# Kernel optimization log

Hardware: AMD Instinct MI355X
Metric: run time of the kernel (lower is better)

Reference implementation:

```python
import jax, jax.numpy as jnp
import numpy as np

DIM = 1024
HEADS = 16
DIM_HEAD = 64
WINDOW = 256  # sliding window size == block size
NEG = -1e9


def rms_norm(x, gamma, size):
    # F.normalize(x, dim=-1) * sqrt(size) * gamma
    nrm = jnp.sqrt(jnp.sum(x * x, axis=-1, keepdims=True))
    return x / jnp.maximum(nrm, 1e-12) * (size ** 0.5) * gamma


def sliding_window_attention(q, k, v, window):
    # q,k,v: [b, h, S, d]; causal local attention: key j valid iff i-window <= j <= i
    b, h, S, d = q.shape
    Bk = window
    nb = S // Bk
    qb = q.reshape(b, h, nb, Bk, d)
    kb = k.reshape(b, h, nb, Bk, d)
    vb = v.reshape(b, h, nb, Bk, d)
    # previous key/value block (zeros for block 0; masked out below)
    k_prev = jnp.pad(kb, ((0, 0), (0, 0), (1, 0), (0, 0), (0, 0)))[:, :, :nb]
    v_prev = jnp.pad(vb, ((0, 0), (0, 0), (1, 0), (0, 0), (0, 0)))[:, :, :nb]
    kctx = jnp.concatenate([k_prev, kb], axis=3)  # [b,h,nb,2Bk,d]
    vctx = jnp.concatenate([v_prev, vb], axis=3)
    scale = 1.0 / jnp.sqrt(jnp.asarray(d, q.dtype))
    scores = jnp.einsum('bhnqd,bhnkd->bhnqk', qb, kctx) * scale  # [b,h,nb,Bk,2Bk]
    qi = jnp.arange(Bk)[:, None]          # local query index
    kj = jnp.arange(2 * Bk)[None, :]      # local key index (offset -Bk rel to block start)
    diff = Bk + qi - kj                   # global i - j
    base = (diff >= 0) & (diff <= window)  # [Bk, 2Bk]
    blk = jnp.arange(nb)[:, None, None]
    key_exists = ((blk - 1) * Bk + kj[None]) >= 0  # [nb,1,2Bk] -> broadcast
    mask = base[None] & key_exists                 # [nb,Bk,2Bk]
    scores = jnp.where(mask[None, None], scores, NEG)
    attn = jax.nn.softmax(scores, axis=-1)
    out = jnp.einsum('bhnqk,bhnkd->bhnqd', attn, vctx)
    return out.reshape(b, h, S, d)


def setup_inputs() -> dict:
    key = jax.random.key(0)
    ks = jax.random.split(key, 6)
    b, S = 2, 4096
    dim_inner = HEADS * DIM_HEAD
    x = jax.random.normal(ks[0], (b, S, DIM), dtype=jnp.float32)
    gamma = jnp.ones((DIM,), dtype=jnp.float32)
    W_qkv = jax.random.normal(ks[1], (DIM, 3 * dim_inner), dtype=jnp.float32) * 0.02
    W_gates = jax.random.normal(ks[2], (DIM, HEADS), dtype=jnp.float32) * 0.02
    b_gates = jnp.zeros((HEADS,), dtype=jnp.float32)
    W_out = jax.random.normal(ks[3], (dim_inner, DIM), dtype=jnp.float32) * 0.02
    return {"x": x, "gamma": gamma, "W_qkv": W_qkv, "W_gates": W_gates,
            "b_gates": b_gates, "W_out": W_out}


def reference(x, gamma, W_qkv, W_gates, b_gates, W_out):
    b, S, dim = x.shape
    xn = rms_norm(x, gamma, dim)
    qkv = xn @ W_qkv                                    # [b,S,3*h*d]
    qkv = qkv.reshape(b, S, 3, HEADS, DIM_HEAD)
    q, k, v = [jnp.transpose(t, (0, 2, 1, 3)) for t in
               (qkv[:, :, 0], qkv[:, :, 1], qkv[:, :, 2])]  # [b,h,S,d]
    out = sliding_window_attention(q, k, v, WINDOW)      # [b,h,S,d]
    gates = xn @ W_gates + b_gates                       # [b,S,h]
    out = out * jax.nn.sigmoid(jnp.transpose(gates, (0, 2, 1)))[..., None]
    out = jnp.transpose(out, (0, 2, 1, 3)).reshape(b, S, HEADS * DIM_HEAD)
    return out @ W_out
```

## Files before the change

### kernel.cpp

```cpp
#include <hip/hip_runtime.h>
#include <hip/hip_bf16.h>
#include <stdint.h>

typedef __bf16 bf16;
typedef __bf16 bf16x4 __attribute__((ext_vector_type(4)));
typedef __bf16 bf16x8 __attribute__((ext_vector_type(8)));
typedef float f32x4 __attribute__((ext_vector_type(4)));

#define GLOBAL_AS __attribute__((address_space(1)))
#define LDS_AS __attribute__((address_space(3)))

__device__ __forceinline__ void g2lds16(const bf16* g, bf16* l) {
  __builtin_amdgcn_global_load_lds((const GLOBAL_AS void*)g, (LDS_AS void*)l, 16, 0, 0);
}

__global__ __launch_bounds__(256) void rmsnorm_kernel(
    const float* __restrict__ x, const float* __restrict__ gamma,
    bf16* __restrict__ xn) {
  __shared__ float wss[4];
  const int t = threadIdx.x;
  const size_t row = blockIdx.x;
  const float* xr = x + row * 1024;

  float4 xv = *(const float4*)&xr[t * 4];
  float v[4] = {xv.x, xv.y, xv.z, xv.w};
  float ss = v[0]*v[0] + v[1]*v[1] + v[2]*v[2] + v[3]*v[3];
#pragma unroll
  for (int mm = 1; mm < 64; mm <<= 1) ss += __shfl_xor(ss, mm);
  if ((t & 63) == 0) wss[t >> 6] = ss;
  __syncthreads();
  ss = wss[0] + wss[1] + wss[2] + wss[3];
  float inv = 32.0f / sqrtf(fmaxf(ss, 1e-24f));

  float4 gv = *(const float4*)&gamma[t * 4];
  float gvv[4] = {gv.x, gv.y, gv.z, gv.w};
  bf16x4 outv;
#pragma unroll
  for (int i = 0; i < 4; ++i) outv[i] = (bf16)(v[i] * inv * gvv[i]);
  *(bf16x4*)&xn[row * 1024 + t * 4] = outv;
}

__global__ void transpose_f32_bf16(const float* __restrict__ in, bf16* __restrict__ out,
                                   int R, int C) {
  __shared__ bf16 tile[32][33];
  const int tx = threadIdx.x, ty = threadIdx.y;
  const int c0 = blockIdx.x * 32, r0 = blockIdx.y * 32;
#pragma unroll
  for (int i = 0; i < 32; i += 8)
    tile[ty + i][tx] = (bf16)in[(size_t)(r0 + ty + i) * C + c0 + tx];
  __syncthreads();
#pragma unroll
  for (int i = 0; i < 32; i += 8)
    out[(size_t)(c0 + ty + i) * R + r0 + tx] = tile[tx][ty + i];
}

__global__ __launch_bounds__(256) void wg_transpose(const float* __restrict__ Wg,
                                                    bf16* __restrict__ BtAug) {
  int idx = blockIdx.x * 256 + threadIdx.x;
  int n = idx >> 10, k = idx & 1023;
  BtAug[(size_t)(3072 + n) * 1024 + k] = (bf16)Wg[(size_t)k * 16 + n];
}

template <typename OutT>
__global__ __launch_bounds__(256) void gemm_bt_128(
    const bf16* __restrict__ A, const bf16* __restrict__ Bt,
    OutT* __restrict__ C, int M, int N, int K) {
  __shared__ bf16 lA[128 * 64];
  __shared__ bf16 lB[128 * 64];
  const int t = threadIdx.x;
  const int w = t >> 6, lane = t & 63;
  const int col0 = lane & 15, quad = lane >> 4;
  const int m0 = blockIdx.y * 128, n0 = blockIdx.x * 128;
  const int wr = (w >> 1) * 64, wc = (w & 1) * 64;

  const int lrow = t >> 3;
  const int sswz = (((t & 7) ^ (lrow & 7)) << 3);

  f32x4 acc[4][4] = {};

  for (int k0 = 0; k0 < K; k0 += 64) {
    __syncthreads();
#pragma unroll
    for (int c = 0; c < 4; ++c) {
      g2lds16(A  + (size_t)(m0 + c * 32 + lrow) * K + k0 + sswz, &lA[c * 2048 + w * 512]);
      g2lds16(Bt + (size_t)(n0 + c * 32 + lrow) * K + k0 + sswz, &lB[c * 2048 + w * 512]);
    }
    __syncthreads();

#pragma unroll
    for (int kh = 0; kh < 2; ++kh) {
      bf16x8 af[4], bfr[4];
#pragma unroll
      for (int i = 0; i < 4; ++i) {
        int row = wr + i * 16 + col0;
        af[i] = *(const bf16x8*)&lA[row * 64 + (((kh * 4 + quad) ^ (row & 7)) << 3)];
      }
#pragma unroll
      for (int j = 0; j < 4; ++j) {
        int row = wc + j * 16 + col0;
        bfr[j] = *(const bf16x8*)&lB[row * 64 + (((kh * 4 + quad) ^ (row & 7)) << 3)];
      }
#pragma unroll
      for (int i = 0; i < 4; ++i)
#pragma unroll
        for (int j = 0; j < 4; ++j)
          acc[i][j] = __builtin_amdgcn_mfma_f32_16x16x32_bf16(af[i], bfr[j], acc[i][j], 0, 0, 0);
    }
  }

#pragma unroll
  for (int i = 0; i < 4; ++i)
#pragma unroll
    for (int j = 0; j < 4; ++j)
#pragma unroll
      for (int r = 0; r < 4; ++r) {
        int row = m0 + wr + i * 16 + quad * 4 + r;
        int col = n0 + wc + j * 16 + col0;
        C[(size_t)row * N + col] = (OutT)acc[i][j][r];
      }
}

template <typename OutT>
__global__ __launch_bounds__(512, 2) void gemm_bt_256(
    const bf16* __restrict__ A, const bf16* __restrict__ Bt,
    OutT* __restrict__ C, int M, int N, int K) {
  extern __shared__ bf16 lds[];
  bf16* A0 = lds;
  bf16* B0 = lds + 16384;
  bf16* A1 = lds + 32768;
  bf16* B1 = lds + 49152;

  const int t = threadIdx.x;
  const int w = t >> 6, lane = t & 63;
  const int wm = w >> 2, wn = w & 3;
  const int col0 = lane & 15, quad = lane >> 4;
  const int sswz = (((t & 7) ^ ((t >> 3) & 7)) << 3);

  int nwg = gridDim.x * gridDim.y;
  int bid = blockIdx.y * gridDim.x + blockIdx.x;
  int swz = bid;
  if ((nwg & 7) == 0) swz = (bid & 7) * (nwg >> 3) + (bid >> 3);
  const int n0 = (swz % gridDim.x) * 256;
  const int m0 = (swz / gridDim.x) * 256;

  const bf16* Abase = A + (size_t)m0 * (size_t)K;

  auto stageA = [&](int ks, int c, bf16* dstA) {
    int row = c * 64 + (t >> 3);
    g2lds16(Abase + (size_t)row * K + ks + sswz, dstA + c * 4096 + w * 512);
  };
  auto stageB = [&](int ks, int c, bf16* dstB) {
    int gr = n0 + c * 64 + (t >> 3);
    gr = (gr < N) ? gr : (N - 1);
    g2lds16(Bt + (size_t)gr * (size_t)K + ks + sswz, dstB + c * 4096 + w * 512);
  };

  f32x4 acc[4][2][4] = {};
  const int NT = K >> 6;

  stageB(0, 0, B0); stageB(0, 1, B0); stageB(0, 2, B0); stageB(0, 3, B0);
  stageA(0, 0, A0);
  stageA(0, 1, A0); stageA(0, 2, A0); stageA(0, 3, A0);
  asm volatile("s_waitcnt vmcnt(3)" ::: "memory");
  __builtin_amdgcn_s_barrier();

  for (int T = 0; T < NT; ++T) {
    bf16* cA = (T & 1) ? A1 : A0;
    bf16* cB = (T & 1) ? B1 : B0;
    bf16* nA = (T & 1) ? A0 : A1;
    bf16* nB = (T & 1) ? B0 : B1;
    int tn = T + 1;
    int kn = ((tn < NT) ? tn : 0) << 6;

    bf16x8 bv[4][2];
#pragma unroll
    for (int q = 0; q < 4; ++q) {
      if (q == 0) {
#pragma unroll
        for (int nj = 0; nj < 4; ++nj) {
          int br = wn * 64 + nj * 16 + col0;
#pragma unroll
          for (int ks = 0; ks < 2; ++ks)
            bv[nj][ks] = *(const bf16x8*)&cB[br * 64 + (((ks * 4 + quad) ^ (br & 7)) << 3)];
        }
      }
      bf16x8 af[2][2];
#pragma unroll
      for (int m2 = 0; m2 < 2; ++m2) {
        int ar = q * 64 + wm * 32 + m2 * 16 + col0;
#pragma unroll
        for (int ks = 0; ks < 2; ++ks)
          af[m2][ks] = *(const bf16x8*)&cA[ar * 64 + (((ks * 4 + quad) ^ (ar & 7)) << 3)];
      }
      if (q == 0)      { stageA(kn, 0, nA); stageB(kn, 0, nB); }
      else if (q == 1) { stageB(kn, 1, nB); stageB(kn, 2, nB); }
      else if (q == 2) { stageB(kn, 3, nB); stageA(kn, 1, nA); }
      else             { stageA(kn, 2, nA); stageA(kn, 3, nA); }
      if (q == 0)      asm volatile("s_waitcnt vmcnt(4)" ::: "memory");
      else if (q == 1) asm volatile("s_waitcnt vmcnt(5)" ::: "memory");
      else if (q == 2) asm volatile("s_waitcnt vmcnt(6)" ::: "memory");
      else             asm volatile("s_waitcnt vmcnt(3)" ::: "memory");
      __builtin_amdgcn_s_barrier();
      asm volatile("s_waitcnt lgkmcnt(0)" ::: "memory");
      __builtin_amdgcn_sched_barrier(0);
      __builtin_amdgcn_s_setprio(1);
#pragma unroll
      for (int ks = 0; ks < 2; ++ks)
#pragma unroll
        for (int m2 = 0; m2 < 2; ++m2)
#pragma unroll
          for (int nj = 0; nj < 4; ++nj)
            acc[q][m2][nj] = __builtin_amdgcn_mfma_f32_16x16x32_bf16(
                af[m2][ks], bv[nj][ks], acc[q][m2][nj], 0, 0, 0);
      __builtin_amdgcn_s_setprio(0);
      __builtin_amdgcn_s_barrier();
    }
  }
  asm volatile("s_waitcnt vmcnt(0)" ::: "memory");

#pragma unroll
  for (int q = 0; q < 4; ++q)
#pragma unroll
    for (int m2 = 0; m2 < 2; ++m2)
#pragma unroll
      for (int nj = 0; nj < 4; ++nj) {
        int col = n0 + wn * 64 + nj * 16 + col0;
        if (col < N) {
          size_t base = (size_t)(m0 + q * 64 + wm * 32 + m2 * 16 + quad * 4) * N + col;
#pragma unroll
          for (int r = 0; r < 4; ++r)
            C[base + (size_t)r * N] = (OutT)acc[q][m2][nj][r];
        }
      }
}

#define NEG_BIG -1e30f
__global__ __launch_bounds__(256, 4) void attn_kernel(
    const bf16* __restrict__ qkv, const float* __restrict__ bg,
    bf16* __restrict__ attnO) {
  __shared__ bf16 lKV[320 * 64];

  const int t = threadIdx.x;
  const int lane = t & 63;
  const int w = t >> 6;
  const int col0 = lane & 15, quad = lane >> 4;

  const int bid = blockIdx.x;
  const int blk = ((bid & 7) << 8) | (bid >> 3);
  const int g = blk & 63;
  const int h = (blk >> 6) & 15;
  const int bb = blk >> 10;
  const int qs = g * 64;

  const size_t rs = 3200;
  const bf16* qbase = qkv + ((size_t)bb * 4096) * rs + h * 64;

  {
    const int lr = t >> 3;
    const int sswz = ((t & 7) ^ (lr & 7)) << 3;
#pragma unroll
    for (int c = 0; c < 10; ++c) {
      int j = qs - 256 + c * 32 + lr;
      j = (j < 0) ? 0 : j;
      g2lds16(qbase + 1024 + (size_t)j * rs + sswz, &lKV[c * 2048 + w * 512]);
    }
  }
  __builtin_amdgcn_sched_barrier(0);
  const int ql = w * 16 + col0;
  const int srow = qs + ql;
  const bf16x8 bq0 = *(const bf16x8*)(qbase + (size_t)srow * rs + quad * 8);
  const bf16x8 bq1 = *(const bf16x8*)(qbase + (size_t)srow * rs + 32 + quad * 8);
  const float logit = (float)qkv[((size_t)bb * 4096 + srow) * rs + 3072 + h];
  asm volatile("s_waitcnt vmcnt(3)" ::: "memory");
  asm volatile("s_barrier" ::: "memory");

  f32x4 z[20];
#pragma unroll
  for (int kt = 0; kt < 20; ++kt) {
    const int kr = kt * 16 + col0;
    bf16x8 a0 = *(const bf16x8*)&lKV[kr * 64 + ((quad ^ (kr & 7)) << 3)];
    bf16x8 a1 = *(const bf16x8*)&lKV[kr * 64 + (((4 + quad) ^ (kr & 7)) << 3)];
    f32x4 zz = {};
    zz = __builtin_amdgcn_mfma_f32_16x16x32_bf16(a0, bq0, zz, 0, 0, 0);
    zz = __builtin_amdgcn_mfma_f32_16x16x32_bf16(a1, bq1, zz, 0, 0, 0);
    z[kt] = zz;
  }
  asm volatile("s_barrier" ::: "memory");

  {
    const int jl = t & 31, dg = t >> 5;
#pragma unroll
    for (int cc = 0; cc < 10; ++cc) {
      int j = qs - 256 + cc * 32 + jl;
      j = (j < 0) ? 0 : j;
      bf16 tmp[8];
      *(uint4*)tmp = *(const uint4*)(qbase + 2048 + (size_t)j * rs + dg * 8);
      const int ck = cc * 4 + (jl >> 3);
      const int wi = jl & 7;
#pragma unroll
      for (int d2 = 0; d2 < 8; ++d2) {
        const int d = dg * 8 + d2;
        lKV[d * 320 + ((ck ^ (d & 7)) << 3) + wi] = tmp[d2];
      }
    }
  }

  float m = NEG_BIG;
#pragma unroll
  for (int kt = 0; kt < 20; ++kt)
#pragma unroll
    for (int r = 0; r < 4; ++r) {
      const int c = kt * 16 + quad * 4 + r;
      const bool valid = (c >= ql) && (c <= ql + 256) && (qs - 256 + c >= 0);
      const float sv = valid ? z[kt][r] * 0.125f : NEG_BIG;
      z[kt][r] = sv;
      m = fmaxf(m, sv);
    }
  m = fmaxf(m, __shfl_xor(m, 16));
  m = fmaxf(m, __shfl_xor(m, 32));
  float l = 0.f;
#pragma unroll
  for (int kt = 0; kt < 20; ++kt)
#pragma unroll
    for (int r = 0; r < 4; ++r) {
      const float p = __expf(z[kt][r] - m);
      z[kt][r] = p;
      l += p;
    }
  l += __shfl_xor(l, 16);
  l += __shfl_xor(l, 32);

  __syncthreads();

  f32x4 o[4] = {};
  const int sl0 = col0 + ((quad & 1) << 5);
  const bool hi = quad >= 2;
#pragma unroll
  for (int kc = 0; kc < 10; ++kc) {
    uint32_t Pl0, Pl1, Ph0, Ph1;
    asm("v_cvt_pk_bf16_f32 %0, %1, %2" : "=v"(Pl0) : "v"(z[2*kc][0]),   "v"(z[2*kc][1]));
    asm("v_cvt_pk_bf16_f32 %0, %1, %2" : "=v"(Pl1) : "v"(z[2*kc][2]),   "v"(z[2*kc][3]));
    asm("v_cvt_pk_bf16_f32 %0, %1, %2" : "=v"(Ph0) : "v"(z[2*kc+1][0]), "v"(z[2*kc+1][1]));
    asm("v_cvt_pk_bf16_f32 %0, %1, %2" : "=v"(Ph1) : "v"(z[2*kc+1][2]), "v"(z[2*kc+1][3]));
    uint32_t w0l = __shfl((int)Pl0, sl0),      w0h = __shfl((int)Ph0, sl0);
    uint32_t w1l = __shfl((int)Pl1, sl0),      w1h = __shfl((int)Ph1, sl0);
    uint32_t w2l = __shfl((int)Pl0, sl0 + 16), w2h = __shfl((int)Ph0, sl0 + 16);
    uint32_t w3l = __shfl((int)Pl1, sl0 + 16), w3h = __shfl((int)Ph1, sl0 + 16);
    union { uint32_t u[4]; bf16x8 v; } pu;
    pu.u[0] = hi ? w0h : w0l;
    pu.u[1] = hi ? w1h : w1l;
    pu.u[2] = hi ? w2h : w2l;
    pu.u[3] = hi ? w3h : w3l;
#pragma unroll
    for (int n = 0; n < 4; ++n) {
      const int d = n * 16 + col0;
      bf16x8 av = *(const bf16x8*)&lKV[d * 320 + (((kc * 4 + quad) ^ (d & 7)) << 3)];
      o[n] = __builtin_amdgcn_mfma_f32_16x16x32_bf16(av, pu.v, o[n], 0, 0, 0);
    }
  }

  const float gate = 1.f / (1.f + __expf(-(logit + bg[h])));
  const float scale = gate / l;
  bf16* obase = attnO + ((size_t)bb * 4096 + srow) * 1024 + h * 64;
#pragma unroll
  for (int n = 0; n < 4; ++n) {
    bf16x4 ov;
#pragma unroll
    for (int r = 0; r < 4; ++r) ov[r] = (bf16)(o[n][r] * scale);
    *(bf16x4*)&obase[n * 16 + quad * 4] = ov;
  }
}

extern "C" void kernel_launch(void* const* d_in, const int* in_sizes, int n_in,
                              void* d_out, int out_size, void* d_ws, size_t ws_size,
                              hipStream_t stream) {
  const float *x = nullptr, *gamma = nullptr, *Wqkv = nullptr,
              *Wg = nullptr, *bg = nullptr, *Wout = nullptr;
  for (int i = 0; i < n_in; ++i) {
    switch (in_sizes[i]) {
      case 8388608: x     = (const float*)d_in[i]; break;
      case 1024:    gamma = (const float*)d_in[i]; break;
      case 3145728: Wqkv  = (const float*)d_in[i]; break;
      case 16384:   Wg    = (const float*)d_in[i]; break;
      case 16:      bg    = (const float*)d_in[i]; break;
      case 1048576: Wout  = (const float*)d_in[i]; break;
    }
  }
  float* out = (float*)d_out;

  static bool attr_done = false;
  if (!attr_done) {
    hipFuncSetAttribute(reinterpret_cast<const void*>(&gemm_bt_256<bf16>),
                        hipFuncAttributeMaxDynamicSharedMemorySize, 131072);
    attr_done = true;
  }

  char* ws = (char*)d_ws;
  bf16* qkv   = (bf16*)ws;  ws += (size_t)8192 * 3200 * 2;
  bf16* xn    = (bf16*)ws;
  bf16* attnO = (bf16*)ws;  ws += (size_t)8192 * 1024 * 2;
  bf16* BtAug = (bf16*)ws;  ws += (size_t)3200 * 1024 * 2;
  bf16* WoutT = (bf16*)ws;  ws += (size_t)1024 * 1024 * 2;

  hipMemsetAsync(BtAug + (size_t)3088 * 1024, 0, (size_t)112 * 1024 * 2, stream);

  rmsnorm_kernel<<<8192, 256, 0, stream>>>(x, gamma, xn);
  transpose_f32_bf16<<<dim3(3072 / 32, 1024 / 32), dim3(32, 8), 0, stream>>>(Wqkv, BtAug, 1024, 3072);
  wg_transpose<<<64, 256, 0, stream>>>(Wg, BtAug);
  transpose_f32_bf16<<<dim3(1024 / 32, 1024 / 32), dim3(32, 8), 0, stream>>>(Wout, WoutT, 1024, 1024);
  gemm_bt_256<bf16><<<dim3(13, 32), 512, 131072, stream>>>(xn, BtAug, qkv, 8192, 3200, 1024);
  attn_kernel<<<2048, 256, 0, stream>>>(qkv, bg, attnO);
  gemm_bt_128<float><<<dim3(1024 / 128, 8192 / 128), 256, 0, stream>>>(attnO, WoutT, out, 8192, 1024, 1024);
}
```

Measured before the change: 235.1 us.

## Load B fragments directly from global to registers, stage only A in LDS

The QKV GEMM no longer stages the B (weight) tile through LDS. Each wave reads its B fragments straight from global memory into registers, and only the A tile stays double-buffered in static LDS (64 KB instead of 128 KB dynamic). This cuts LDS footprint and LDS traffic for B, drops per-quarter barriers, and simplifies the pipeline to one wait and barrier per K step. The trade-off is uncached-by-LDS global loads for B, which are redundantly read by waves sharing columns, and a full vmcnt(0) wait that exposes load latency.

```diff
diff --git a/kernel.cpp b/kernel.cpp
--- a/kernel.cpp
+++ b/kernel.cpp
@@ -124,11 +124,7 @@
 __global__ __launch_bounds__(512, 2) void gemm_bt_256(
     const bf16* __restrict__ A, const bf16* __restrict__ Bt,
     OutT* __restrict__ C, int M, int N, int K) {
-  extern __shared__ bf16 lds[];
-  bf16* A0 = lds;
-  bf16* B0 = lds + 16384;
-  bf16* A1 = lds + 32768;
-  bf16* B1 = lds + 49152;
+  __shared__ bf16 lA[2][256 * 64];
 
   const int t = threadIdx.x;
   const int w = t >> 6, lane = t & 63;
@@ -149,60 +145,51 @@
     int row = c * 64 + (t >> 3);
     g2lds16(Abase + (size_t)row * K + ks + sswz, dstA + c * 4096 + w * 512);
   };
-  auto stageB = [&](int ks, int c, bf16* dstB) {
-    int gr = n0 + c * 64 + (t >> 3);
+
+  const bf16* brow[4];
+#pragma unroll
+  for (int nj = 0; nj < 4; ++nj) {
+    int gr = n0 + wn * 64 + nj * 16 + col0;
     gr = (gr < N) ? gr : (N - 1);
-    g2lds16(Bt + (size_t)gr * (size_t)K + ks + sswz, dstB + c * 4096 + w * 512);
-  };
+    brow[nj] = Bt + (size_t)gr * (size_t)K + quad * 8;
+  }
 
   f32x4 acc[4][2][4] = {};
   const int NT = K >> 6;
 
-  stageB(0, 0, B0); stageB(0, 1, B0); stageB(0, 2, B0); stageB(0, 3, B0);
-  stageA(0, 0, A0);
-  stageA(0, 1, A0); stageA(0, 2, A0); stageA(0, 3, A0);
-  asm volatile("s_waitcnt vmcnt(3)" ::: "memory");
-  __builtin_amdgcn_s_barrier();
+  stageA(0, 0, lA[0]); stageA(0, 1, lA[0]); stageA(0, 2, lA[0]); stageA(0, 3, lA[0]);
 
   for (int T = 0; T < NT; ++T) {
-    bf16* cA = (T & 1) ? A1 : A0;
-    bf16* cB = (T & 1) ? B1 : B0;
-    bf16* nA = (T & 1) ? A0 : A1;
-    bf16* nB = (T & 1) ? B0 : B1;
-    int tn = T + 1;
-    int kn = ((tn < NT) ? tn : 0) << 6;
+    bf16* cur = lA[T & 1];
+    bf16* nxt = lA[(T + 1) & 1];
+    const int k0 = T << 6;
+
+    asm volatile("s_waitcnt vmcnt(0)" ::: "memory");
+    asm volatile("s_barrier" ::: "memory");
 
     bf16x8 bv[4][2];
 #pragma unroll
+    for (int nj = 0; nj < 4; ++nj)
+#pragma unroll
+      for (int ks = 0; ks < 2; ++ks)
+        bv[nj][ks] = *(const bf16x8*)(brow[nj] + k0 + ks * 32);
+    __builtin_amdgcn_sched_barrier(0);
+
+    if (T + 1 < NT) {
+      const int kn = (T + 1) << 6;
+      stageA(kn, 0, nxt); stageA(kn, 1, nxt); stageA(kn, 2, nxt); stageA(kn, 3, nxt);
+    }
+
+#pragma unroll
     for (int q = 0; q < 4; ++q) {
-      if (q == 0) {
-#pragma unroll
-        for (int nj = 0; nj < 4; ++nj) {
-          int br = wn * 64 + nj * 16 + col0;
-#pragma unroll
-          for (int ks = 0; ks < 2; ++ks)
-            bv[nj][ks] = *(const bf16x8*)&cB[br * 64 + (((ks * 4 + quad) ^ (br & 7)) << 3)];
-        }
-      }
       bf16x8 af[2][2];
 #pragma unroll
       for (int m2 = 0; m2 < 2; ++m2) {
         int ar = q * 64 + wm * 32 + m2 * 16 + col0;
 #pragma unroll
         for (int ks = 0; ks < 2; ++ks)
-          af[m2][ks] = *(const bf16x8*)&cA[ar * 64 + (((ks * 4 + quad) ^ (ar & 7)) << 3)];
-      }
-      if (q == 0)      { stageA(kn, 0, nA); stageB(kn, 0, nB); }
-      else if (q == 1) { stageB(kn, 1, nB); stageB(kn, 2, nB); }
-      else if (q == 2) { stageB(kn, 3, nB); stageA(kn, 1, nA); }
-      else             { stageA(kn, 2, nA); stageA(kn, 3, nA); }
-      if (q == 0)      asm volatile("s_waitcnt vmcnt(4)" ::: "memory");
-      else if (q == 1) asm volatile("s_waitcnt vmcnt(5)" ::: "memory");
-      else if (q == 2) asm volatile("s_waitcnt vmcnt(6)" ::: "memory");
-      else             asm volatile("s_waitcnt vmcnt(3)" ::: "memory");
-      __builtin_amdgcn_s_barrier();
-      asm volatile("s_waitcnt lgkmcnt(0)" ::: "memory");
-      __builtin_amdgcn_sched_barrier(0);
+          af[m2][ks] = *(const bf16x8*)&cur[ar * 64 + (((ks * 4 + quad) ^ (ar & 7)) << 3)];
+      }
       __builtin_amdgcn_s_setprio(1);
 #pragma unroll
       for (int ks = 0; ks < 2; ++ks)
@@ -213,7 +200,6 @@
             acc[q][m2][nj] = __builtin_amdgcn_mfma_f32_16x16x32_bf16(
                 af[m2][ks], bv[nj][ks], acc[q][m2][nj], 0, 0, 0);
       __builtin_amdgcn_s_setprio(0);
-      __builtin_amdgcn_s_barrier();
     }
   }
   asm volatile("s_waitcnt vmcnt(0)" ::: "memory");
@@ -388,13 +374,6 @@
   }
   float* out = (float*)d_out;
 
-  static bool attr_done = false;
-  if (!attr_done) {
-    hipFuncSetAttribute(reinterpret_cast<const void*>(&gemm_bt_256<bf16>),
-                        hipFuncAttributeMaxDynamicSharedMemorySize, 131072);
-    attr_done = true;
-  }
-
   char* ws = (char*)d_ws;
   bf16* qkv   = (bf16*)ws;  ws += (size_t)8192 * 3200 * 2;
   bf16* xn    = (bf16*)ws;
@@ -408,7 +387,7 @@
   transpose_f32_bf16<<<dim3(3072 / 32, 1024 / 32), dim3(32, 8), 0, stream>>>(Wqkv, BtAug, 1024, 3072);
   wg_transpose<<<64, 256, 0, stream>>>(Wg, BtAug);
   transpose_f32_bf16<<<dim3(1024 / 32, 1024 / 32), dim3(32, 8), 0, stream>>>(Wout, WoutT, 1024, 1024);
-  gemm_bt_256<bf16><<<dim3(13, 32), 512, 131072, stream>>>(xn, BtAug, qkv, 8192, 3200, 1024);
+  gemm_bt_256<bf16><<<dim3(13, 32), 512, 0, stream>>>(xn, BtAug, qkv, 8192, 3200, 1024);
   attn_kernel<<<2048, 256, 0, stream>>>(qkv, bg, attnO);
   gemm_bt_128<float><<<dim3(1024 / 128, 8192 / 128), 256, 0, stream>>>(attnO, WoutT, out, 8192, 1024, 1024);
 }
```

After: 270.5 us. 15.0% more time.

## Replace output GEMM with pipelined 256x128 kernel and restructure QKV GEMM warp tiling

Applied to the files above, without the earlier changes.

Drops the simple 128x128 output-projection GEMM in favour of a new 256x128, 512-thread kernel with double-buffered direct-to-LDS loads, grid swizzling and staged vmcnt waits. The QKV GEMM's warp layout changes so each warp owns 128 rows by 64 columns instead of four 32-row strips, with new per-warp staging addresses and the K loop unrolled by two over the buffers. The aim is better data reuse and overlap of global loads with MFMA work. The hand-placed waitcnt and barrier ordering is delicate and could add stalls or produce wrong results if the counts are off.

```diff
diff --git a/kernel.cpp b/kernel.cpp
--- a/kernel.cpp
+++ b/kernel.cpp
@@ -59,65 +59,6 @@
   int idx = blockIdx.x * 256 + threadIdx.x;
   int n = idx >> 10, k = idx & 1023;
   BtAug[(size_t)(3072 + n) * 1024 + k] = (bf16)Wg[(size_t)k * 16 + n];
-}
-
-template <typename OutT>
-__global__ __launch_bounds__(256) void gemm_bt_128(
-    const bf16* __restrict__ A, const bf16* __restrict__ Bt,
-    OutT* __restrict__ C, int M, int N, int K) {
-  __shared__ bf16 lA[128 * 64];
-  __shared__ bf16 lB[128 * 64];
-  const int t = threadIdx.x;
-  const int w = t >> 6, lane = t & 63;
-  const int col0 = lane & 15, quad = lane >> 4;
-  const int m0 = blockIdx.y * 128, n0 = blockIdx.x * 128;
-  const int wr = (w >> 1) * 64, wc = (w & 1) * 64;
-
-  const int lrow = t >> 3;
-  const int sswz = (((t & 7) ^ (lrow & 7)) << 3);
-
-  f32x4 acc[4][4] = {};
-
-  for (int k0 = 0; k0 < K; k0 += 64) {
-    __syncthreads();
-#pragma unroll
-    for (int c = 0; c < 4; ++c) {
-      g2lds16(A  + (size_t)(m0 + c * 32 + lrow) * K + k0 + sswz, &lA[c * 2048 + w * 512]);
-      g2lds16(Bt + (size_t)(n0 + c * 32 + lrow) * K + k0 + sswz, &lB[c * 2048 + w * 512]);
-    }
-    __syncthreads();
-
-#pragma unroll
-    for (int kh = 0; kh < 2; ++kh) {
-      bf16x8 af[4], bfr[4];
-#pragma unroll
-      for (int i = 0; i < 4; ++i) {
-        int row = wr + i * 16 + col0;
-        af[i] = *(const bf16x8*)&lA[row * 64 + (((kh * 4 + quad) ^ (row & 7)) << 3)];
-      }
-#pragma unroll
-      for (int j = 0; j < 4; ++j) {
-        int row = wc + j * 16 + col0;
-        bfr[j] = *(const bf16x8*)&lB[row * 64 + (((kh * 4 + quad) ^ (row & 7)) << 3)];
-      }
-#pragma unroll
-      for (int i = 0; i < 4; ++i)
-#pragma unroll
-        for (int j = 0; j < 4; ++j)
-          acc[i][j] = __builtin_amdgcn_mfma_f32_16x16x32_bf16(af[i], bfr[j], acc[i][j], 0, 0, 0);
-    }
-  }
-
-#pragma unroll
-  for (int i = 0; i < 4; ++i)
-#pragma unroll
-    for (int j = 0; j < 4; ++j)
-#pragma unroll
-      for (int r = 0; r < 4; ++r) {
-        int row = m0 + wr + i * 16 + quad * 4 + r;
-        int col = n0 + wc + j * 16 + col0;
-        C[(size_t)row * N + col] = (OutT)acc[i][j][r];
-      }
 }
 
 template <typename OutT>
@@ -134,7 +75,8 @@
   const int w = t >> 6, lane = t & 63;
   const int wm = w >> 2, wn = w & 3;
   const int col0 = lane & 15, quad = lane >> 4;
-  const int sswz = (((t & 7) ^ ((t >> 3) & 7)) << 3);
+  const int s_sub = lane >> 3;
+  const int sswz = (((lane & 7) ^ s_sub) << 3);
 
   int nwg = gridDim.x * gridDim.y;
   int bid = blockIdx.y * gridDim.x + blockIdx.x;
@@ -146,19 +88,155 @@
   const bf16* Abase = A + (size_t)m0 * (size_t)K;
 
   auto stageA = [&](int ks, int c, bf16* dstA) {
+    int rb = (w < 4) ? (c * 32 + w * 8) : (128 + c * 32 + (w - 4) * 8);
+    g2lds16(Abase + (size_t)(rb + s_sub) * K + ks + sswz, dstA + rb * 64);
+  };
+  auto stageB = [&](int ks, int c, bf16* dstB) {
+    int rb = c * 64 + w * 8;
+    int gr = n0 + rb + s_sub;
+    gr = (gr < N) ? gr : (N - 1);
+    g2lds16(Bt + (size_t)gr * (size_t)K + ks + sswz, dstB + rb * 64);
+  };
+
+  f32x4 acc[8][4] = {};
+  const int NT = K >> 6;
+  const int NI = NT >> 1;
+
+#pragma unroll
+  for (int c = 0; c < 4; ++c) stageB(0, c, B0);
+  stageA(0, 0, A0);
+  stageA(0, 1, A0); stageA(0, 2, A0); stageA(0, 3, A0);
+  asm volatile("s_waitcnt vmcnt(3)" ::: "memory");
+  __builtin_amdgcn_s_barrier();
+
+  for (int i = 0; i < NI; ++i) {
+#pragma unroll
+    for (int h = 0; h < 2; ++h) {
+      bf16* cA = h ? A1 : A0;
+      bf16* cB = h ? B1 : B0;
+      bf16* nA = h ? A0 : A1;
+      bf16* nB = h ? B0 : B1;
+      int tn = 2 * i + h + 1;
+      int kn = ((tn < NT) ? tn : 0) << 6;
+
+      bf16x8 bv[4][2];
+#pragma unroll
+      for (int nj = 0; nj < 4; ++nj) {
+        int br = wn * 64 + nj * 16 + col0;
+#pragma unroll
+        for (int ks = 0; ks < 2; ++ks)
+          bv[nj][ks] = *(const bf16x8*)&cB[br * 64 + (((ks * 4 + quad) ^ (br & 7)) << 3)];
+      }
+      {
+        bf16x8 af[2][2];
+#pragma unroll
+        for (int m2 = 0; m2 < 2; ++m2) {
+          int ar = wm * 128 + m2 * 16 + col0;
+#pragma unroll
+          for (int ks = 0; ks < 2; ++ks)
+            af[m2][ks] = *(const bf16x8*)&cA[ar * 64 + (((ks * 4 + quad) ^ (ar & 7)) << 3)];
+        }
+        stageB(kn, 0, nB); stageB(kn, 1, nB);
+        __builtin_amdgcn_s_barrier();
+        asm volatile("s_waitcnt lgkmcnt(0)" ::: "memory");
+        __builtin_amdgcn_s_setprio(1);
+#pragma unroll
+        for (int ks = 0; ks < 2; ++ks)
+#pragma unroll
+          for (int m2 = 0; m2 < 2; ++m2)
+#pragma unroll
+            for (int nj = 0; nj < 4; ++nj)
+              acc[m2][nj] = __builtin_amdgcn_mfma_f32_16x16x32_bf16(
+                  af[m2][ks], bv[nj][ks], acc[m2][nj], 0, 0, 0);
+        __builtin_amdgcn_s_setprio(0);
+        asm volatile("s_waitcnt vmcnt(4)" ::: "memory");
+        __builtin_amdgcn_s_barrier();
+      }
+
+#pragma unroll
+      for (int p = 1; p < 4; ++p) {
+        bf16x8 af[2][2];
+#pragma unroll
+        for (int m2 = 0; m2 < 2; ++m2) {
+          int ar = wm * 128 + (p * 2 + m2) * 16 + col0;
+#pragma unroll
+          for (int ks = 0; ks < 2; ++ks)
+            af[m2][ks] = *(const bf16x8*)&cA[ar * 64 + (((ks * 4 + quad) ^ (ar & 7)) << 3)];
+        }
+        if (p == 1)      { stageB(kn, 2, nB); stageB(kn, 3, nB); stageA(kn, 0, nA); }
+        else if (p == 2) { stageA(kn, 1, nA); stageA(kn, 2, nA); }
+        else             { stageA(kn, 3, nA); }
+        __builtin_amdgcn_s_barrier();
+        asm volatile("s_waitcnt lgkmcnt(0)" ::: "memory");
+        __builtin_amdgcn_s_setprio(1);
+#pragma unroll
+        for (int ks = 0; ks < 2; ++ks)
+#pragma unroll
+          for (int m2 = 0; m2 < 2; ++m2)
+#pragma unroll
+            for (int nj = 0; nj < 4; ++nj)
+              acc[p * 2 + m2][nj] = __builtin_amdgcn_mfma_f32_16x16x32_bf16(
+                  af[m2][ks], bv[nj][ks], acc[p * 2 + m2][nj], 0, 0, 0);
+        __builtin_amdgcn_s_setprio(0);
+        if (p == 1)      asm volatile("s_waitcnt vmcnt(6)" ::: "memory");
+        else if (p == 2) asm volatile("s_waitcnt vmcnt(7)" ::: "memory");
+        else             asm volatile("s_waitcnt vmcnt(3)" ::: "memory");
+        __builtin_amdgcn_s_barrier();
+      }
+    }
+  }
+  asm volatile("s_waitcnt vmcnt(0)" ::: "memory");
+
+#pragma unroll
+  for (int mi = 0; mi < 8; ++mi)
+#pragma unroll
+    for (int nj = 0; nj < 4; ++nj) {
+      int col = n0 + wn * 64 + nj * 16 + col0;
+      if (col < N) {
+        size_t base = (size_t)(m0 + wm * 128 + mi * 16 + quad * 4) * N + col;
+#pragma unroll
+        for (int r = 0; r < 4; ++r)
+          C[base + (size_t)r * N] = (OutT)acc[mi][nj][r];
+      }
+    }
+}
+
+__global__ __launch_bounds__(512, 2) void gemm_out_256x128(
+    const bf16* __restrict__ A, const bf16* __restrict__ Bt,
+    float* __restrict__ C, int M, int N, int K) {
+  extern __shared__ bf16 lds[];
+  bf16* A0 = lds;
+  bf16* B0 = lds + 16384;
+  bf16* A1 = lds + 24576;
+  bf16* B1 = lds + 40960;
+
+  const int t = threadIdx.x;
+  const int w = t >> 6, lane = t & 63;
+  const int wm = w >> 2, wn = w & 3;
+  const int col0 = lane & 15, quad = lane >> 4;
+  const int sswz = (((t & 7) ^ ((t >> 3) & 7)) << 3);
+
+  int nwg = gridDim.x * gridDim.y;
+  int bid = blockIdx.y * gridDim.x + blockIdx.x;
+  int swz = (bid & 7) * (nwg >> 3) + (bid >> 3);
+  const int n0 = (swz % gridDim.x) * 128;
+  const int m0 = (swz / gridDim.x) * 256;
+
+  const bf16* Abase = A + (size_t)m0 * (size_t)K;
+
+  auto stageA = [&](int ks, int c, bf16* dstA) {
     int row = c * 64 + (t >> 3);
     g2lds16(Abase + (size_t)row * K + ks + sswz, dstA + c * 4096 + w * 512);
   };
   auto stageB = [&](int ks, int c, bf16* dstB) {
     int gr = n0 + c * 64 + (t >> 3);
-    gr = (gr < N) ? gr : (N - 1);
     g2lds16(Bt + (size_t)gr * (size_t)K + ks + sswz, dstB + c * 4096 + w * 512);
   };
 
-  f32x4 acc[4][2][4] = {};
+  f32x4 acc[8][2] = {};
   const int NT = K >> 6;
 
-  stageB(0, 0, B0); stageB(0, 1, B0); stageB(0, 2, B0); stageB(0, 3, B0);
+  stageB(0, 0, B0); stageB(0, 1, B0);
   stageA(0, 0, A0);
   stageA(0, 1, A0); stageA(0, 2, A0); stageA(0, 3, A0);
   asm volatile("s_waitcnt vmcnt(3)" ::: "memory");
@@ -169,16 +247,16 @@
     bf16* cB = (T & 1) ? B1 : B0;
     bf16* nA = (T & 1) ? A0 : A1;
     bf16* nB = (T & 1) ? B0 : B1;
-    int tn = T + 1;
-    int kn = ((tn < NT) ? tn : 0) << 6;
-
-    bf16x8 bv[4][2];
-#pragma unroll
-    for (int q = 0; q < 4; ++q) {
-      if (q == 0) {
-#pragma unroll
-        for (int nj = 0; nj < 4; ++nj) {
-          int br = wn * 64 + nj * 16 + col0;
+    const int tn = T + 1;
+    const int kn = ((tn < NT) ? tn : 0) << 6;
+
+    bf16x8 bv[2][2];
+#pragma unroll
+    for (int p = 0; p < 4; ++p) {
+      if (p == 0) {
+#pragma unroll
+        for (int nj = 0; nj < 2; ++nj) {
+          int br = wn * 32 + nj * 16 + col0;
 #pragma unroll
           for (int ks = 0; ks < 2; ++ks)
             bv[nj][ks] = *(const bf16x8*)&cB[br * 64 + (((ks * 4 + quad) ^ (br & 7)) << 3)];
@@ -187,51 +265,44 @@
       bf16x8 af[2][2];
 #pragma unroll
       for (int m2 = 0; m2 < 2; ++m2) {
-        int ar = q * 64 + wm * 32 + m2 * 16 + col0;
+        int ar = wm * 128 + (p * 2 + m2) * 16 + col0;
 #pragma unroll
         for (int ks = 0; ks < 2; ++ks)
           af[m2][ks] = *(const bf16x8*)&cA[ar * 64 + (((ks * 4 + quad) ^ (ar & 7)) << 3)];
       }
-      if (q == 0)      { stageA(kn, 0, nA); stageB(kn, 0, nB); }
-      else if (q == 1) { stageB(kn, 1, nB); stageB(kn, 2, nB); }
-      else if (q == 2) { stageB(kn, 3, nB); stageA(kn, 1, nA); }
+      if (p == 0)      { stageB(kn, 0, nB); stageB(kn, 1, nB); }
+      else if (p == 1) { stageA(kn, 0, nA); }
+      else if (p == 2) { stageA(kn, 1, nA); }
       else             { stageA(kn, 2, nA); stageA(kn, 3, nA); }
-      if (q == 0)      asm volatile("s_waitcnt vmcnt(4)" ::: "memory");
-      else if (q == 1) asm volatile("s_waitcnt vmcnt(5)" ::: "memory");
-      else if (q == 2) asm volatile("s_waitcnt vmcnt(6)" ::: "memory");
-      else             asm volatile("s_waitcnt vmcnt(3)" ::: "memory");
       __builtin_amdgcn_s_barrier();
       asm volatile("s_waitcnt lgkmcnt(0)" ::: "memory");
-      __builtin_amdgcn_sched_barrier(0);
       __builtin_amdgcn_s_setprio(1);
 #pragma unroll
       for (int ks = 0; ks < 2; ++ks)
 #pragma unroll
         for (int m2 = 0; m2 < 2; ++m2)
 #pragma unroll
-          for (int nj = 0; nj < 4; ++nj)
-            acc[q][m2][nj] = __builtin_amdgcn_mfma_f32_16x16x32_bf16(
-                af[m2][ks], bv[nj][ks], acc[q][m2][nj], 0, 0, 0);
+          for (int nj = 0; nj < 2; ++nj)
+            acc[p * 2 + m2][nj] = __builtin_amdgcn_mfma_f32_16x16x32_bf16(
+                af[m2][ks], bv[nj][ks], acc[p * 2 + m2][nj], 0, 0, 0);
       __builtin_amdgcn_s_setprio(0);
+      if (p == 3) asm volatile("s_waitcnt vmcnt(3)" ::: "memory");
+      else        asm volatile("s_waitcnt vmcnt(4)" ::: "memory");
       __builtin_amdgcn_s_barrier();
     }
   }
   asm volatile("s_waitcnt vmcnt(0)" ::: "memory");
 
 #pragma unroll
-  for (int q = 0; q < 4; ++q)
-#pragma unroll
-    for (int m2 = 0; m2 < 2; ++m2)
-#pragma unroll
-      for (int nj = 0; nj < 4; ++nj) {
-        int col = n0 + wn * 64 + nj * 16 + col0;
-        if (col < N) {
-          size_t base = (size_t)(m0 + q * 64 + wm * 32 + m2 * 16 + quad * 4) * N + col;
-#pragma unroll
-          for (int r = 0; r < 4; ++r)
-            C[base + (size_t)r * N] = (OutT)acc[q][m2][nj][r];
-        }
-      }
+  for (int mi = 0; mi < 8; ++mi)
+#pragma unroll
+    for (int nj = 0; nj < 2; ++nj) {
+      int col = n0 + wn * 32 + nj * 16 + col0;
+      size_t base = (size_t)(m0 + wm * 128 + mi * 16 + quad * 4) * N + col;
+#pragma unroll
+      for (int r = 0; r < 4; ++r)
+        C[base + (size_t)r * N] = acc[mi][nj][r];
+    }
 }
 
 #define NEG_BIG -1e30f
@@ -392,6 +463,8 @@
   if (!attr_done) {
     hipFuncSetAttribute(reinterpret_cast<const void*>(&gemm_bt_256<bf16>),
                         hipFuncAttributeMaxDynamicSharedMemorySize, 131072);
+    hipFuncSetAttribute(reinterpret_cast<const void*>(&gemm_out_256x128),
+                        hipFuncAttributeMaxDynamicSharedMemorySize, 98304);
     attr_done = true;
   }
 
@@ -410,5 +483,5 @@
   transpose_f32_bf16<<<dim3(1024 / 32, 1024 / 32), dim3(32, 8), 0, stream>>>(Wout, WoutT, 1024, 1024);
   gemm_bt_256<bf16><<<dim3(13, 32), 512, 131072, stream>>>(xn, BtAug, qkv, 8192, 3200, 1024);
   attn_kernel<<<2048, 256, 0, stream>>>(qkv, bg, attnO);
-  gemm_bt_128<float><<<dim3(1024 / 128, 8192 / 128), 256, 0, stream>>>(attnO, WoutT, out, 8192, 1024, 1024);
-}
+  gemm_out_256x128<<<dim3(8, 32), 512, 98304, stream>>>(attnO, WoutT, out, 8192, 1024, 1024);
+}
```

New measurement: 232.5 us. No clear change (-1.1%).
